# Performance work log

Measured on AMD Instinct MI355X. Metric: run time of the kernel, lower is better.

## Reference

```python
import jax, jax.numpy as jnp
import numpy as np

NUM_SCALES = 3      # num_scales
SPARSITY = 5        # base_sparsity (neighbors per scale)
DT = 0.1
HALF_DT = DT / 2.0
CG_ITERS = 20       # cg_max_iter
CG_TOL = 1e-6       # cg_tol


def ham_matvec(v, w):
    """Multi-scale sparse (stencil) Hamiltonian matvec along last dim.
    H = sum_{m,j} w[m,j] * (2 I - shift(+off) - shift(-off)), off = 2^m * (j+1).
    Real symmetric -> Cayley step is unitary."""
    out = jnp.zeros_like(v)
    for m in range(NUM_SCALES):
        for j in range(SPARSITY):
            off = (2 ** m) * (j + 1)
            out = out + w[m, j] * (2.0 * v - jnp.roll(v, off, axis=-1) - jnp.roll(v, -off, axis=-1))
    return out


def a_minus(x, w):
    """(I + i*dt/2*H) in real-block form. x: [B,S,D,2]."""
    vr, vi = x[..., 0], x[..., 1]
    Hvr = ham_matvec(vr, w)
    Hvi = ham_matvec(vi, w)
    return jnp.stack([vr - HALF_DT * Hvi, vi + HALF_DT * Hvr], axis=-1)


def _dot(a, b):
    # per-(B,S) system inner product over (D, 2)
    return jnp.sum(a * b, axis=(-2, -1))


def cg_solve(w, b):
    """Batched CG solve a_minus(x) = b with x0 = 0, fixed iteration count with
    per-system convergence masking (frozen once residual < tol * ||b||)."""
    x = jnp.zeros_like(b)
    r = b              # b - A(0)
    p = r
    rs = _dot(r, r)    # [B, S]
    thresh = (CG_TOL ** 2) * jnp.maximum(rs, 1e-30)

    def body(carry, _):
        x, r, p, rs = carry
        active = rs > thresh
        Ap = a_minus(p, w)
        alpha = jnp.where(active, rs / (_dot(p, Ap) + 1e-30), 0.0)
        x = x + alpha[..., None, None] * p
        r = r - alpha[..., None, None] * Ap
        rs_new = _dot(r, r)
        beta = jnp.where(active, rs_new / (rs + 1e-30), 0.0)
        p = jnp.where(active[..., None, None], r + beta[..., None, None] * p, p)
        rs = jnp.where(active, rs_new, rs)
        return (x, r, p, rs), None

    (x, _, _, _), _ = jax.lax.scan(body, (x, r, p, rs), None, length=CG_ITERS)
    return x


def setup_inputs() -> dict:
    key = jax.random.key(0)
    k1, k2, k3 = jax.random.split(key, 3)
    B, S, D = 8, 2048, 1024
    psi_r = jax.random.normal(k1, (B, S, D), dtype=jnp.float32)
    psi_i = jax.random.normal(k2, (B, S, D), dtype=jnp.float32)
    alpha = 0.1 * jnp.ones((D,), dtype=jnp.float32)               # nonlinear_alpha init
    ham_w = 0.1 * jax.random.uniform(k3, (NUM_SCALES, SPARSITY), dtype=jnp.float32) + 0.01
    return {"psi_r": psi_r, "psi_i": psi_i, "alpha": alpha, "ham_w": ham_w}


def reference(psi_r, psi_i, alpha, ham_w):
    # nonlinear phase rotation: exp(i * alpha * |psi|^2 / mean|psi|^2)
    intensity = psi_r * psi_r + psi_i * psi_i
    intensity = intensity / (jnp.mean(intensity, axis=-1, keepdims=True) + 1e-8)
    phase = alpha * intensity
    c, s = jnp.cos(phase), jnp.sin(phase)
    rot_r = psi_r * c - psi_i * s
    rot_i = psi_r * s + psi_i * c
    # rhs = (I - i*dt/2*H) psi_rot  (real-block form)
    Hr = ham_matvec(rot_r, ham_w)
    Hi = ham_matvec(rot_i, ham_w)
    rhs = jnp.stack([rot_r + HALF_DT * Hi, rot_i - HALF_DT * Hr], axis=-1)  # [B,S,D,2]
    # Cayley: psi_out = (I + i*dt/2*H)^{-1} rhs via CG
    return cg_solve(ham_w, rhs)
```

## Files before the change

kernel.cpp:

```cpp
#include <hip/hip_runtime.h>
#include <utility>

typedef float v2f __attribute__((ext_vector_type(2)));

#define HDT 0.05f
#define KSTEPS 5

__device__ __forceinline__ float bf2f(unsigned int u) {
    return __uint_as_float(u << 16);
}
__device__ __forceinline__ unsigned int f2bf(float x) {
    unsigned int b = __float_as_uint(x);
    return (b + 0x7FFFu + ((b >> 16) & 1u)) >> 16;
}
__device__ __forceinline__ float rfl(float x) {
    return __int_as_float(__builtin_amdgcn_readfirstlane(__float_as_int(x)));
}

template <int... Is, class F>
__device__ __forceinline__ void static_for_impl(std::integer_sequence<int, Is...>, F&& f) {
    (f(std::integral_constant<int, Is>{}), ...);
}
template <int N, class F>
__device__ __forceinline__ void static_for(F&& f) {
    static_for_impl(std::make_integer_sequence<int, N>{}, (F&&)f);
}

__host__ __device__ constexpr int cidx(int d) {
    int a = d < 0 ? -d : d;
    return (a==0)?0:(a==1)?1:(a==2)?2:(a==3)?3:(a==4)?4:(a==5)?5:(a==6)?6:
           (a==8)?7:(a==10)?8:(a==12)?9:(a==16)?10:(a==20)?11:-1;
}

__global__ void detect_dtype(const unsigned int* __restrict__ w, int* __restrict__ flag) {
    int cnt = 0;
    for (int i = threadIdx.x; i < 4096; i += 64) {
        unsigned int e = (w[i] >> 7) & 0xFFu;
        cnt += (e >= 0x78u && e <= 0x82u) ? 1 : 0;
    }
    #pragma unroll
    for (int off = 32; off; off >>= 1) cnt += __shfl_xor(cnt, off, 64);
    if (threadIdx.x == 0) *flag = (cnt > 2048) ? 1 : 0;
}

__global__ __launch_bounds__(256, 3)
void cayley_main(const void* __restrict__ psi_r, const void* __restrict__ psi_i,
                 const void* __restrict__ alpha, const void* __restrict__ ham_w,
                 void* __restrict__ out, const int* __restrict__ flagp)
{
    __shared__ float4 lds4[2048];

    const int lane = threadIdx.x & 63;
    const int wv   = threadIdx.x >> 6;
    const int sys  = (blockIdx.x << 2) + wv;
    const int sysq = wv << 9;

    const bool isbf = (*flagp) != 0;

    float hw[15];
    if (isbf) {
        const unsigned short* p = (const unsigned short*)ham_w;
        #pragma unroll
        for (int i = 0; i < 15; ++i) hw[i] = bf2f((unsigned int)p[i]);
    } else {
        const float* p = (const float*)ham_w;
        #pragma unroll
        for (int i = 0; i < 15; ++i) hw[i] = p[i];
    }
    float cs[12];
    {
        float s = 0.f;
        #pragma unroll
        for (int i = 0; i < 15; ++i) s += hw[i];
        cs[0]  = rfl( 2.f*HDT*s);
        cs[1]  = rfl(-HDT* hw[0]);
        cs[2]  = rfl(-HDT*(hw[1]+hw[5]));
        cs[3]  = rfl(-HDT* hw[2]);
        cs[4]  = rfl(-HDT*(hw[3]+hw[6]+hw[10]));
        cs[5]  = rfl(-HDT* hw[4]);
        cs[6]  = rfl(-HDT* hw[7]);
        cs[7]  = rfl(-HDT*(hw[8]+hw[11]));
        cs[8]  = rfl(-HDT* hw[9]);
        cs[9]  = rfl(-HDT* hw[12]);
        cs[10] = rfl(-HDT* hw[13]);
        cs[11] = rfl(-HDT* hw[14]);
    }

    int raddr[28];
    #pragma unroll
    for (int g = 0; g < 28; ++g) {
        int qd = (8*lane - 10 + g) & 511;
        raddr[g] = sysq + (qd ^ ((qd >> 3) & 7));
    }
    int waddr[8];
    #pragma unroll
    for (int k = 0; k < 8; ++k) {
        int qd = 8*lane + k;
        waddr[k] = sysq + (qd ^ ((qd >> 3) & 7));
    }

    float pr[16], pq[16], al[16];
    if (isbf) {
        const unsigned short* bR = (const unsigned short*)psi_r + (size_t)sys*1024 + lane*16;
        const unsigned short* bI = (const unsigned short*)psi_i + (size_t)sys*1024 + lane*16;
        const unsigned short* bA = (const unsigned short*)alpha  + lane*16;
        static_for<2>([&](auto hI) {
            constexpr int h = hI.value;
            uint4 a = ((const uint4*)bR)[h];
            uint4 b = ((const uint4*)bI)[h];
            uint4 c = ((const uint4*)bA)[h];
            pr[h*8+0]=bf2f(a.x&0xFFFFu); pr[h*8+1]=bf2f(a.x>>16);
            pr[h*8+2]=bf2f(a.y&0xFFFFu); pr[h*8+3]=bf2f(a.y>>16);
            pr[h*8+4]=bf2f(a.z&0xFFFFu); pr[h*8+5]=bf2f(a.z>>16);
            pr[h*8+6]=bf2f(a.w&0xFFFFu); pr[h*8+7]=bf2f(a.w>>16);
            pq[h*8+0]=bf2f(b.x&0xFFFFu); pq[h*8+1]=bf2f(b.x>>16);
            pq[h*8+2]=bf2f(b.y&0xFFFFu); pq[h*8+3]=bf2f(b.y>>16);
            pq[h*8+4]=bf2f(b.z&0xFFFFu); pq[h*8+5]=bf2f(b.z>>16);
            pq[h*8+6]=bf2f(b.w&0xFFFFu); pq[h*8+7]=bf2f(b.w>>16);
            al[h*8+0]=bf2f(c.x&0xFFFFu); al[h*8+1]=bf2f(c.x>>16);
            al[h*8+2]=bf2f(c.y&0xFFFFu); al[h*8+3]=bf2f(c.y>>16);
            al[h*8+4]=bf2f(c.z&0xFFFFu); al[h*8+5]=bf2f(c.z>>16);
            al[h*8+6]=bf2f(c.w&0xFFFFu); al[h*8+7]=bf2f(c.w>>16);
        });
    } else {
        const float* fR = (const float*)psi_r + (size_t)sys*1024 + lane*16;
        const float* fI = (const float*)psi_i + (size_t)sys*1024 + lane*16;
        const float* fA = (const float*)alpha  + lane*16;
        static_for<4>([&](auto hI) {
            constexpr int h = hI.value;
            float4 a = ((const float4*)fR)[h];
            float4 b = ((const float4*)fI)[h];
            float4 c = ((const float4*)fA)[h];
            pr[4*h]=a.x; pr[4*h+1]=a.y; pr[4*h+2]=a.z; pr[4*h+3]=a.w;
            pq[4*h]=b.x; pq[4*h+1]=b.y; pq[4*h+2]=b.z; pq[4*h+3]=b.w;
            al[4*h]=c.x; al[4*h+1]=c.y; al[4*h+2]=c.z; al[4*h+3]=c.w;
        });
    }

    float ssum = 0.f;
    #pragma unroll
    for (int k = 0; k < 16; ++k) ssum += pr[k]*pr[k] + pq[k]*pq[k];
    #pragma unroll
    for (int off = 32; off; off >>= 1) ssum += __shfl_xor(ssum, off, 64);
    const float inv = 1.f / (ssum * (1.f/1024.f) + 1e-8f);

    v2f cur[16];
    static_for<16>([&](auto kI) {
        constexpr int k = kI.value;
        float inten = (pr[k]*pr[k] + pq[k]*pq[k]) * inv;
        float ph = al[k] * inten;
        float cc = __cosf(ph), sn = __sinf(ph);
        cur[k].x = pr[k]*cc - pq[k]*sn;
        cur[k].y = pr[k]*sn + pq[k]*cc;
    });

    v2f acc[16], b[16], t[16];

    auto ldswrite = [&](v2f (&arr)[16]) {
        static_for<8>([&](auto kI) {
            constexpr int k8 = kI.value;
            lds4[waddr[k8]] = make_float4(arr[2*k8].x, arr[2*k8].y,
                                          arr[2*k8+1].x, arr[2*k8+1].y);
        });
    };
    auto stencil = [&]() {
        static_for<16>([&](auto kI) { acc[kI.value].x = 0.f; acc[kI.value].y = 0.f; });
        static_for<28>([&](auto gI) {
            constexpr int g = gI.value;
            float4 q = lds4[raddr[g]];
            v2f e0; e0.x = q.x; e0.y = q.y;
            v2f e1; e1.x = q.z; e1.y = q.w;
            static_for<16>([&](auto kI) {
                constexpr int k = kI.value;
                constexpr int id0 = cidx(2*g     - 20 - k);
                constexpr int id1 = cidx(2*g + 1 - 20 - k);
                if constexpr (id0 >= 0) acc[k] += cs[id0] * e0;
                if constexpr (id1 >= 0) acc[k] += cs[id1] * e1;
            });
        });
    };

    ldswrite(cur);
    stencil();
    static_for<16>([&](auto kI) {
        constexpr int k = kI.value;
        b[k].x = cur[k].x + acc[k].y;
        b[k].y = cur[k].y - acc[k].x;
    });
    ldswrite(b);

    #pragma unroll 1
    for (int itn = 0; itn < KSTEPS; ++itn) {
        stencil();
        static_for<16>([&](auto kI) {
            constexpr int k = kI.value;
            t[k].x = b[k].x + acc[k].y;
            t[k].y = b[k].y - acc[k].x;
        });
        if (itn != KSTEPS - 1) ldswrite(t);
    }

    if (isbf) {
        unsigned short* po = (unsigned short*)out + (size_t)sys*2048 + lane*32;
        uint4* po4 = (uint4*)po;
        static_for<4>([&](auto hI) {
            constexpr int h = hI.value;
            uint4 v;
            v.x = f2bf(t[4*h+0].x) | (f2bf(t[4*h+0].y) << 16);
            v.y = f2bf(t[4*h+1].x) | (f2bf(t[4*h+1].y) << 16);
            v.z = f2bf(t[4*h+2].x) | (f2bf(t[4*h+2].y) << 16);
            v.w = f2bf(t[4*h+3].x) | (f2bf(t[4*h+3].y) << 16);
            po4[h] = v;
        });
    } else {
        float* po = (float*)out + (size_t)sys*2048 + lane*32;
        static_for<8>([&](auto kI) {
            constexpr int k8 = kI.value;
            *(float4*)(po + 4*k8) = make_float4(t[2*k8].x, t[2*k8].y,
                                                t[2*k8+1].x, t[2*k8+1].y);
        });
    }
}

extern "C" void kernel_launch(void* const* d_in, const int* in_sizes, int n_in,
                              void* d_out, int out_size, void* d_ws, size_t ws_size,
                              hipStream_t stream)
{
    (void)in_sizes; (void)n_in; (void)out_size; (void)ws_size;
    detect_dtype<<<dim3(1), dim3(64), 0, stream>>>((const unsigned int*)d_in[0], (int*)d_ws);
    cayley_main<<<dim3(4096), dim3(256), 0, stream>>>(d_in[0], d_in[1], d_in[2], d_in[3],
                                                      d_out, (const int*)d_ws);
}
```

Baseline: 302.2 us.

## Use padded per-lane LDS layout with halo copies and constant-offset stencil reads

Replaces the XOR-swizzled circular LDS layout with a padded linear layout (one pad slot every 8 float4s, 600 slots per system). The 10-element wrap-around halo is written twice, once at each end, so every stencil read is a compile-time offset from a per-lane base pointer. This drops the 28 precomputed read addresses and should free registers, while adding conditional halo stores. It also lowers launch_bounds occupancy from 3 to 2 blocks and shrinks the dtype-detection kernel to a single vectorized load.

```diff
diff --git a/kernel.cpp b/kernel.cpp
--- a/kernel.cpp
+++ b/kernel.cpp
@@ -5,6 +5,8 @@
 
 #define HDT 0.05f
 #define KSTEPS 5
+
+#define SYS_SLOTS 600
 
 __device__ __forceinline__ float bf2f(unsigned int u) {
     return __uint_as_float(u << 16);
@@ -32,28 +34,32 @@
            (a==8)?7:(a==10)?8:(a==12)?9:(a==16)?10:(a==20)?11:-1;
 }
 
-__global__ void detect_dtype(const unsigned int* __restrict__ w, int* __restrict__ flag) {
+__global__ void detect_dtype(const uint4* __restrict__ w, int* __restrict__ flag) {
+    uint4 v = w[threadIdx.x];
     int cnt = 0;
-    for (int i = threadIdx.x; i < 4096; i += 64) {
-        unsigned int e = (w[i] >> 7) & 0xFFu;
+    unsigned int ws[4] = {v.x, v.y, v.z, v.w};
+    #pragma unroll
+    for (int i = 0; i < 4; ++i) {
+        unsigned int e = (ws[i] >> 7) & 0xFFu;
         cnt += (e >= 0x78u && e <= 0x82u) ? 1 : 0;
     }
     #pragma unroll
     for (int off = 32; off; off >>= 1) cnt += __shfl_xor(cnt, off, 64);
-    if (threadIdx.x == 0) *flag = (cnt > 2048) ? 1 : 0;
-}
-
-__global__ __launch_bounds__(256, 3)
+    if (threadIdx.x == 0) *flag = (cnt > 128) ? 1 : 0;
+}
+
+__global__ __launch_bounds__(256, 2)
 void cayley_main(const void* __restrict__ psi_r, const void* __restrict__ psi_i,
                  const void* __restrict__ alpha, const void* __restrict__ ham_w,
                  void* __restrict__ out, const int* __restrict__ flagp)
 {
-    __shared__ float4 lds4[2048];
+    __shared__ float4 lds4[4 * SYS_SLOTS];
 
     const int lane = threadIdx.x & 63;
     const int wv   = threadIdx.x >> 6;
     const int sys  = (blockIdx.x << 2) + wv;
-    const int sysq = wv << 9;
+    float4* const sl   = lds4 + wv * SYS_SLOTS;
+    float4* const base = sl + 9 * lane;
 
     const bool isbf = (*flagp) != 0;
 
@@ -86,17 +92,14 @@
         cs[11] = rfl(-HDT* hw[14]);
     }
 
-    int raddr[28];
-    #pragma unroll
-    for (int g = 0; g < 28; ++g) {
-        int qd = (8*lane - 10 + g) & 511;
-        raddr[g] = sysq + (qd ^ ((qd >> 3) & 7));
-    }
-    int waddr[8];
+    int hoff[8];
     #pragma unroll
     for (int k = 0; k < 8; ++k) {
         int qd = 8*lane + k;
-        waddr[k] = sysq + (qd ^ ((qd >> 3) & 7));
+        int h = -1;
+        if (qd < 10)  { int idx = qd + 522; h = idx + (idx >> 3); }
+        if (qd >= 502){ int idx = qd - 502; h = idx + (idx >> 3); }
+        hoff[k] = h;
     }
 
     float pr[16], pq[16], al[16];
@@ -158,22 +161,26 @@
 
     auto ldswrite = [&](v2f (&arr)[16]) {
         static_for<8>([&](auto kI) {
-            constexpr int k8 = kI.value;
-            lds4[waddr[k8]] = make_float4(arr[2*k8].x, arr[2*k8].y,
-                                          arr[2*k8+1].x, arr[2*k8+1].y);
+            constexpr int k = kI.value;
+            constexpr int woff = (k <= 5) ? (11 + k) : (12 + k);
+            float4 val = make_float4(arr[2*k].x, arr[2*k].y,
+                                     arr[2*k+1].x, arr[2*k+1].y);
+            base[woff] = val;
+            if (hoff[k] >= 0) sl[hoff[k]] = val;
         });
     };
     auto stencil = [&]() {
         static_for<16>([&](auto kI) { acc[kI.value].x = 0.f; acc[kI.value].y = 0.f; });
-        static_for<28>([&](auto gI) {
-            constexpr int g = gI.value;
-            float4 q = lds4[raddr[g]];
+        static_for<28>([&](auto cI) {
+            constexpr int c = cI.value;
+            constexpr int roff = c + (c >> 3);
+            float4 q = base[roff];
             v2f e0; e0.x = q.x; e0.y = q.y;
             v2f e1; e1.x = q.z; e1.y = q.w;
             static_for<16>([&](auto kI) {
                 constexpr int k = kI.value;
-                constexpr int id0 = cidx(2*g     - 20 - k);
-                constexpr int id1 = cidx(2*g + 1 - 20 - k);
+                constexpr int id0 = cidx(2*c     - 20 - k);
+                constexpr int id1 = cidx(2*c + 1 - 20 - k);
                 if constexpr (id0 >= 0) acc[k] += cs[id0] * e0;
                 if constexpr (id1 >= 0) acc[k] += cs[id1] * e1;
             });
@@ -227,7 +234,7 @@
                               hipStream_t stream)
 {
     (void)in_sizes; (void)n_in; (void)out_size; (void)ws_size;
-    detect_dtype<<<dim3(1), dim3(64), 0, stream>>>((const unsigned int*)d_in[0], (int*)d_ws);
+    detect_dtype<<<dim3(1), dim3(64), 0, stream>>>((const uint4*)d_in[0], (int*)d_ws);
     cayley_main<<<dim3(4096), dim3(256), 0, stream>>>(d_in[0], d_in[1], d_in[2], d_in[3],
                                                       d_out, (const int*)d_ws);
 }
```

Result: slower. 308.3 us (+2.0%).
